# Kernel tuning notes

Hardware: AMD Instinct MI355X
Metric: run time of the kernel (lower is better)

## Reference

```python
import jax, jax.numpy as jnp
import numpy as np

M_COMP = 8      # number of output components m (n = m * tmax)
TMAX = 512
BS = 32
N = M_COMP * TMAX  # 4096


def setup_inputs() -> dict:
    key = jax.random.key(0)
    k1, k2, k3, k4 = jax.random.split(key, 4)
    # K must be symmetric positive definite for the Cholesky factorization.
    A = jax.random.normal(k1, (N, N), dtype=jnp.float32)
    K = A @ A.T / N + 1e-2 * jnp.eye(N, dtype=jnp.float32)
    # Sigma: diagonal measurement-noise covariance (positive diagonal).
    Sigma = jnp.diag(jax.random.uniform(k2, (N,), dtype=jnp.float32, minval=0.1, maxval=0.5))
    mu = jax.random.normal(k3, (N,), dtype=jnp.float32)
    Y = jax.random.normal(k4, (BS * N,), dtype=jnp.float32)
    return {"Y": Y, "mu": mu, "K": K, "Sigma": Sigma, "bs": BS, "tmax": TMAX}


def reference(Y, mu, K, Sigma, bs, tmax):
    n = mu.shape[0]  # m * tmax
    KS = K + Sigma
    # Chol_inv: inv = L^{-T} L^{-1} = (K + Sigma)^{-1}
    L = jnp.linalg.cholesky(KS)
    Linv = jnp.linalg.inv(L)
    inv = Linv.T @ Linv  # [n, n]
    # Block-diagonal quadratic form == sum of per-trajectory quadratic forms.
    diff = mu[None, :] - Y.reshape(bs, n)  # [bs, n]
    quad = jnp.einsum('bi,ij,bj->', diff, inv, diff)
    # log det(K + Sigma); slogdet is the stable equivalent (det > 0 for SPD).
    _, logdet = jnp.linalg.slogdet(KS)
    lml = (-quad / (2.0 * bs)
           - 0.5 * logdet
           - 0.5 * tmax * jnp.log(jnp.asarray(2.0 * np.pi, dtype=KS.dtype)))
    return -lml
```

## Files before the change

kernel.cpp:

```cpp
#include <hip/hip_runtime.h>
#include <math.h>

#define Nn 4096
#define BSc 32
#define NB 128
#define NBP 132
#define NBB 32
#define NBLK 33
#define NK 32
#define TILE_ELEMS (NB * NB)
#define NTILES 561

typedef float f32x4 __attribute__((ext_vector_type(4)));
typedef short bf16x8 __attribute__((ext_vector_type(8)));

__device__ __forceinline__ size_t tile_off(int i, int j) {
  return ((size_t)(j * NBLK - (j * (j - 1)) / 2 + (i - j))) * TILE_ELEMS;
}

__device__ __forceinline__ unsigned short f2bf(float f) {
  union { float f; unsigned int u; } v; v.f = f;
  unsigned int r = v.u + 0x7fffu + ((v.u >> 16) & 1u);
  return (unsigned short)(r >> 16);
}
__device__ __forceinline__ float bf2f(unsigned short b) {
  union { unsigned int u; float f; } v; v.u = ((unsigned int)b) << 16;
  return v.f;
}

__global__ __launch_bounds__(256) void prep(const float* __restrict__ Y,
                                            const float* __restrict__ mu,
                                            const float* __restrict__ Kp,
                                            const float* __restrict__ Sg,
                                            float* __restrict__ W) {
  int bid = blockIdx.x;
  int j = 0;
  while (j + 1 < NBLK) {
    int nxt = (j + 1) * NBLK - ((j + 1) * j) / 2;
    if (bid < nxt) break;
    ++j;
  }
  int start = j * NBLK - (j * (j - 1)) / 2;
  int i = j + (bid - start);
  float* T = W + tile_off(i, j);
  int tid = threadIdx.x;
  for (int idx = tid; idx < TILE_ELEMS; idx += 256) {
    int li = idx >> 7, lj = idx & 127;
    int gr = i * NB + li, gc = j * NB + lj;
    float v = 0.0f;
    if (gr < Nn) {
      v = Kp[(size_t)gr * Nn + gc];
      if (gr == gc) v += Sg[(size_t)gr * Nn + gr];
    } else {
      int b = gr - Nn;
      if (b < BSc && gc < Nn) v = mu[gc] - Y[(size_t)b * Nn + gc];
    }
    T[idx] = v;
  }
}

__global__ __launch_bounds__(256) void potf2(float* __restrict__ W, int k) {
  __shared__ float T[NB][NBP];
  __shared__ float dinv_sh[NBB];
  float* G = W + tile_off(k, k);
  int tid = threadIdx.x;
  for (int idx = tid; idx < TILE_ELEMS / 4; idx += 256) {
    float4 v = ((const float4*)G)[idx];
    int r = idx >> 5, c = (idx & 31) * 4;
    *(float4*)&T[r][c] = v;
  }
  __syncthreads();
  int lane = tid & 63, wid = tid >> 6;
#pragma unroll 1
  for (int kb = 0; kb < 4; ++kb) {
    int o = kb * NBB;
    if (wid == 0) {
      int ii = lane & 31;
      float cc[NBB];
#pragma unroll
      for (int p = 0; p < NBB; ++p) cc[p] = T[o + ii][o + p];
#pragma unroll
      for (int j = 0; j < NBB; ++j) {
        float s = cc[j];
#pragma unroll
        for (int p = 0; p < NBB; ++p) {
          if (p < j) s -= cc[p] * __shfl(cc[p], j, 64);
        }
        float sj = __shfl(s, j, 64);
        float d = sqrtf(sj);
        if (ii == j) cc[j] = d;
        else if (ii > j) cc[j] = s / d;
      }
      if (lane < 32) {
#pragma unroll
        for (int p = 0; p < NBB; ++p) {
          if (p <= ii) T[o + ii][o + p] = cc[p];
        }
      }
    }
    __syncthreads();
    if (tid < NBB) dinv_sh[tid] = 1.0f / T[o + tid][o + tid];
    __syncthreads();
    int R = NB - o - NBB;
    if (R > 0) {
      if (tid < R) {
        int r = o + NBB + tid;
        float x[NBB];
#pragma unroll
        for (int p4 = 0; p4 < 8; ++p4) {
          float4 v = *(const float4*)&T[r][o + p4 * 4];
          x[p4 * 4] = v.x; x[p4 * 4 + 1] = v.y; x[p4 * 4 + 2] = v.z; x[p4 * 4 + 3] = v.w;
        }
#pragma unroll
        for (int j = 0; j < NBB; ++j) {
          float s = x[j];
#pragma unroll
          for (int p = 0; p < NBB; ++p) {
            if (p < j) s -= x[p] * T[o + j][o + p];
          }
          x[j] = s * dinv_sh[j];
        }
#pragma unroll
        for (int c4 = 0; c4 < 8; ++c4) {
          float4 w; w.x = x[c4 * 4]; w.y = x[c4 * 4 + 1]; w.z = x[c4 * 4 + 2]; w.w = x[c4 * 4 + 3];
          *(float4*)&T[r][o + c4 * 4] = w;
        }
      }
      __syncthreads();
      int TL = R >> 2;
      int ntile = TL * (TL + 1) / 2;
#pragma unroll 1
      for (int t = tid; t < ntile; t += 256) {
        int ti = (int)((sqrtf(8.0f * t + 1.0f) - 1.0f) * 0.5f);
        while ((ti + 1) * (ti + 2) / 2 <= t) ++ti;
        while (ti * (ti + 1) / 2 > t) --ti;
        int tj = t - ti * (ti + 1) / 2;
        int tr = o + NBB + ti * 4, tc = o + NBB + tj * 4;
        float acc[4][4];
#pragma unroll
        for (int m = 0; m < 4; ++m)
#pragma unroll
          for (int n = 0; n < 4; ++n) acc[m][n] = 0.0f;
#pragma unroll
        for (int p4 = 0; p4 < 8; ++p4) {
          float4 a[4], b[4];
#pragma unroll
          for (int m = 0; m < 4; ++m) a[m] = *(const float4*)&T[tr + m][o + p4 * 4];
#pragma unroll
          for (int n = 0; n < 4; ++n) b[n] = *(const float4*)&T[tc + n][o + p4 * 4];
#pragma unroll
          for (int m = 0; m < 4; ++m)
#pragma unroll
            for (int n = 0; n < 4; ++n)
              acc[m][n] += a[m].x * b[n].x + a[m].y * b[n].y + a[m].z * b[n].z + a[m].w * b[n].w;
        }
#pragma unroll
        for (int m = 0; m < 4; ++m)
#pragma unroll
          for (int n = 0; n < 4; ++n) T[tr + m][tc + n] -= acc[m][n];
      }
    }
    __syncthreads();
  }
  for (int idx = tid; idx < TILE_ELEMS; idx += 256) {
    int i = idx >> 7, j = idx & 127;
    if (j <= i) G[idx] = T[i][j];
  }
}

__global__ __launch_bounds__(256) void trsm(float* __restrict__ W,
                                            unsigned short* __restrict__ PH,
                                            unsigned short* __restrict__ PL,
                                            int k) {
  __shared__ float Td[NB][NBP];
  __shared__ float X[NB][NBP];
  __shared__ float dinv_sh[NB];
  int tid = threadIdx.x;
  int i = k + 1 + blockIdx.x;
  int rows = (i == NBLK - 1) ? BSc : NB;
  const float* Gd = W + tile_off(k, k);
  const float* Gx = W + tile_off(i, k);
  for (int idx = tid; idx < TILE_ELEMS / 4; idx += 256) {
    float4 v = ((const float4*)Gd)[idx];
    float4 u = ((const float4*)Gx)[idx];
    int r = idx >> 5, c = (idx & 31) * 4;
    *(float4*)&Td[r][c] = v;
    if (r >= rows) { u.x = 0.0f; u.y = 0.0f; u.z = 0.0f; u.w = 0.0f; }
    *(float4*)&X[r][c] = u;
  }
  __syncthreads();
  if (tid < NB) dinv_sh[tid] = 1.0f / Td[tid][tid];
  __syncthreads();
  int rtile = (tid >> 3) * 4;
  int ctile = (tid & 7) * 4;
#pragma unroll 1
  for (int jb = 0; jb < 4; ++jb) {
    int o = jb * NBB;
    if (jb > 0) {
      float acc[4][4];
#pragma unroll
      for (int m = 0; m < 4; ++m)
#pragma unroll
        for (int n = 0; n < 4; ++n) acc[m][n] = 0.0f;
#pragma unroll 1
      for (int p4 = 0; p4 < (o >> 2); ++p4) {
        float4 a[4], b[4];
#pragma unroll
        for (int m = 0; m < 4; ++m) a[m] = *(const float4*)&X[rtile + m][p4 * 4];
#pragma unroll
        for (int n = 0; n < 4; ++n) b[n] = *(const float4*)&Td[o + ctile + n][p4 * 4];
#pragma unroll
        for (int m = 0; m < 4; ++m)
#pragma unroll
          for (int n = 0; n < 4; ++n)
            acc[m][n] += a[m].x * b[n].x + a[m].y * b[n].y + a[m].z * b[n].z + a[m].w * b[n].w;
      }
#pragma unroll
      for (int m = 0; m < 4; ++m)
#pragma unroll
        for (int n = 0; n < 4; ++n) X[rtile + m][o + ctile + n] -= acc[m][n];
      __syncthreads();
    }
    if (tid < NB) {
      int r = tid;
      float x[NBB];
#pragma unroll
      for (int p4 = 0; p4 < 8; ++p4) {
        float4 v = *(const float4*)&X[r][o + p4 * 4];
        x[p4 * 4] = v.x; x[p4 * 4 + 1] = v.y; x[p4 * 4 + 2] = v.z; x[p4 * 4 + 3] = v.w;
      }
#pragma unroll
      for (int j = 0; j < NBB; ++j) {
        float s = x[j];
#pragma unroll
        for (int p = 0; p < NBB; ++p) {
          if (p < j) s -= x[p] * Td[o + j][o + p];
        }
        x[j] = s * dinv_sh[o + j];
      }
#pragma unroll
      for (int c4 = 0; c4 < 8; ++c4) {
        float4 w; w.x = x[c4 * 4]; w.y = x[c4 * 4 + 1]; w.z = x[c4 * 4 + 2]; w.w = x[c4 * 4 + 3];
        *(float4*)&X[r][o + c4 * 4] = w;
      }
    }
    __syncthreads();
  }
  int r = tid >> 1, hf = tid & 1;
  unsigned short* ph = PH + (size_t)i * TILE_ELEMS + (size_t)r * NB + hf * 64;
  unsigned short* pl = PL + (size_t)i * TILE_ELEMS + (size_t)r * NB + hf * 64;
#pragma unroll 1
  for (int ch = 0; ch < 8; ++ch) {
    unsigned short hb[8], lb[8];
#pragma unroll
    for (int e = 0; e < 8; ++e) {
      float v = X[r][hf * 64 + ch * 8 + e];
      unsigned short h = f2bf(v);
      hb[e] = h;
      lb[e] = f2bf(v - bf2f(h));
    }
    *reinterpret_cast<uint4*>(&ph[ch * 8]) = *reinterpret_cast<const uint4*>(hb);
    *reinterpret_cast<uint4*>(&pl[ch * 8]) = *reinterpret_cast<const uint4*>(lb);
  }
}

__global__ __launch_bounds__(256) void syrk(const unsigned short* __restrict__ PH,
                                            const unsigned short* __restrict__ PL,
                                            float* __restrict__ W, int k) {
  int i = k + 1 + blockIdx.x, j = k + 1 + blockIdx.y;
  if (i < j) return;
  const unsigned short* Ahg = PH + (size_t)i * TILE_ELEMS;
  const unsigned short* Alg = PL + (size_t)i * TILE_ELEMS;
  const unsigned short* Bhg = PH + (size_t)j * TILE_ELEMS;
  const unsigned short* Blg = PL + (size_t)j * TILE_ELEMS;
  float* C = W + tile_off(i, j);
  __shared__ unsigned short Ah[NB][40], Al[NB][40], Bh[NB][40], Bl[NB][40];
  int tid = threadIdx.x, lane = tid & 63, wid = tid >> 6;
  int wr = wid >> 1, wc = wid & 1, lm = lane & 15, lk = lane >> 4;
  f32x4 acc[4][4];
#pragma unroll
  for (int m = 0; m < 4; ++m)
#pragma unroll
    for (int n = 0; n < 4; ++n) acc[m][n] = (f32x4)0.0f;
  int r = tid >> 1, hf = tid & 1;
#pragma unroll 1
  for (int kb = 0; kb < 4; ++kb) {
    int kbase = kb * 32;
    if (kb) __syncthreads();
#pragma unroll
    for (int c = 0; c < 2; ++c) {
      int lc = (hf * 2 + c) * 8;
      int kc = kbase + lc;
      *reinterpret_cast<uint4*>(&Ah[r][lc]) = *reinterpret_cast<const uint4*>(&Ahg[(size_t)r * NB + kc]);
      *reinterpret_cast<uint4*>(&Al[r][lc]) = *reinterpret_cast<const uint4*>(&Alg[(size_t)r * NB + kc]);
      *reinterpret_cast<uint4*>(&Bh[r][lc]) = *reinterpret_cast<const uint4*>(&Bhg[(size_t)r * NB + kc]);
      *reinterpret_cast<uint4*>(&Bl[r][lc]) = *reinterpret_cast<const uint4*>(&Blg[(size_t)r * NB + kc]);
    }
    __syncthreads();
    bf16x8 ah[4], al[4], bh[4], bl[4];
#pragma unroll
    for (int mt = 0; mt < 4; ++mt) {
      int row = wr * 64 + mt * 16 + lm;
      ah[mt] = *reinterpret_cast<const bf16x8*>(&Ah[row][lk * 8]);
      al[mt] = *reinterpret_cast<const bf16x8*>(&Al[row][lk * 8]);
    }
#pragma unroll
    for (int nt = 0; nt < 4; ++nt) {
      int col = wc * 64 + nt * 16 + lm;
      bh[nt] = *reinterpret_cast<const bf16x8*>(&Bh[col][lk * 8]);
      bl[nt] = *reinterpret_cast<const bf16x8*>(&Bl[col][lk * 8]);
    }
#pragma unroll
    for (int mt = 0; mt < 4; ++mt)
#pragma unroll
      for (int nt = 0; nt < 4; ++nt) {
        acc[mt][nt] = __builtin_amdgcn_mfma_f32_16x16x32_bf16(ah[mt], bh[nt], acc[mt][nt], 0, 0, 0);
        acc[mt][nt] = __builtin_amdgcn_mfma_f32_16x16x32_bf16(al[mt], bh[nt], acc[mt][nt], 0, 0, 0);
        acc[mt][nt] = __builtin_amdgcn_mfma_f32_16x16x32_bf16(ah[mt], bl[nt], acc[mt][nt], 0, 0, 0);
      }
  }
#pragma unroll
  for (int mt = 0; mt < 4; ++mt)
#pragma unroll
    for (int nt = 0; nt < 4; ++nt) {
#pragma unroll
      for (int q = 0; q < 4; ++q) {
        int rr = wr * 64 + mt * 16 + lk * 4 + q;
        int cc = wc * 64 + nt * 16 + lm;
        C[rr * NB + cc] -= acc[mt][nt][q];
      }
    }
}

__global__ __launch_bounds__(256) void finalize(const float* __restrict__ W,
                                                const int* __restrict__ bsp,
                                                const int* __restrict__ tmaxp,
                                                float* __restrict__ out) {
  __shared__ float rl[4], rq[4];
  int tid = threadIdx.x;
  float lsum = 0.0f;
  for (int d = tid; d < Nn; d += 256) {
    int db = d >> 7, dl = d & 127;
    lsum += logf(W[tile_off(db, db) + (size_t)dl * NB + dl]);
  }
  float qsum = 0.0f;
  if (tid < BSc) qsum = W[tile_off(NBLK - 1, NBLK - 1) + (size_t)tid * NB + tid];
  for (int o = 32; o > 0; o >>= 1) {
    lsum += __shfl_down(lsum, o, 64);
    qsum += __shfl_down(qsum, o, 64);
  }
  int lane = tid & 63, wid = tid >> 6;
  if (lane == 0) { rl[wid] = lsum; rq[wid] = qsum; }
  __syncthreads();
  if (tid == 0) {
    float Lt = rl[0] + rl[1] + rl[2] + rl[3];
    float Qt = rq[0] + rq[1] + rq[2] + rq[3];
    float bsf = (float)bsp[0];
    float tmaxf = (float)tmaxp[0];
    out[0] = -Qt / (2.0f * bsf) + Lt + 0.5f * tmaxf * logf(6.283185307179586f);
  }
}

extern "C" void kernel_launch(void* const* d_in, const int* in_sizes, int n_in,
                              void* d_out, int out_size, void* d_ws, size_t ws_size,
                              hipStream_t stream) {
  const float* Y   = (const float*)d_in[0];
  const float* mu  = (const float*)d_in[1];
  const float* Kp  = (const float*)d_in[2];
  const float* Sg  = (const float*)d_in[3];
  const int*   bsp = (const int*)d_in[4];
  const int*   tmp_= (const int*)d_in[5];
  float* W = (float*)d_ws;
  unsigned short* PH = (unsigned short*)(W + (size_t)NTILES * TILE_ELEMS);
  unsigned short* PL = PH + (size_t)NBLK * TILE_ELEMS;
  float* out = (float*)d_out;

  prep<<<NTILES, 256, 0, stream>>>(Y, mu, Kp, Sg, W);

  for (int k = 0; k < NK; ++k) {
    potf2<<<1, 256, 0, stream>>>(W, k);
    int T = NBLK - (k + 1);
    trsm<<<T, 256, 0, stream>>>(W, PH, PL, k);
    dim3 g(T, T);
    syrk<<<g, 256, 0, stream>>>(PH, PL, W, k);
  }
  finalize<<<1, 256, 0, stream>>>(W, bsp, tmp_, out);
}
```

Measured before the change: 3.917 ms.

## Fuse next diagonal-block Cholesky into the syrk block that updates it

New measurement: 3.696 ms, median of 2. 1.06x faster.

```diff
diff --git a/kernel.cpp b/kernel.cpp
--- a/kernel.cpp
+++ b/kernel.cpp
@@ -10,6 +10,9 @@
 #define NK 32
 #define TILE_ELEMS (NB * NB)
 #define NTILES 561
+
+#define SM_DINV 67584
+#define SM_SIZE 67712
 
 typedef float f32x4 __attribute__((ext_vector_type(4)));
 typedef short bf16x8 __attribute__((ext_vector_type(8)));
@@ -59,17 +62,8 @@
   }
 }
 
-__global__ __launch_bounds__(256) void potf2(float* __restrict__ W, int k) {
-  __shared__ float T[NB][NBP];
-  __shared__ float dinv_sh[NBB];
-  float* G = W + tile_off(k, k);
-  int tid = threadIdx.x;
-  for (int idx = tid; idx < TILE_ELEMS / 4; idx += 256) {
-    float4 v = ((const float4*)G)[idx];
-    int r = idx >> 5, c = (idx & 31) * 4;
-    *(float4*)&T[r][c] = v;
-  }
-  __syncthreads();
+__device__ __forceinline__ void factor_lds(float (*T)[NBP], float* dinv_sh,
+                                           int tid) {
   int lane = tid & 63, wid = tid >> 6;
 #pragma unroll 1
   for (int kb = 0; kb < 4; ++kb) {
@@ -162,6 +156,21 @@
     }
     __syncthreads();
   }
+}
+
+__global__ __launch_bounds__(256) void potf2(float* __restrict__ W, int k) {
+  __shared__ __align__(16) unsigned char SMEM[SM_SIZE];
+  float (*T)[NBP] = (float (*)[NBP])SMEM;
+  float* dinv_sh = (float*)(SMEM + SM_DINV);
+  float* G = W + tile_off(k, k);
+  int tid = threadIdx.x;
+  for (int idx = tid; idx < TILE_ELEMS / 4; idx += 256) {
+    float4 v = ((const float4*)G)[idx];
+    int r = idx >> 5, c = (idx & 31) * 4;
+    *(float4*)&T[r][c] = v;
+  }
+  __syncthreads();
+  factor_lds(T, dinv_sh, tid);
   for (int idx = tid; idx < TILE_ELEMS; idx += 256) {
     int i = idx >> 7, j = idx & 127;
     if (j <= i) G[idx] = T[i][j];
@@ -269,12 +278,16 @@
                                             float* __restrict__ W, int k) {
   int i = k + 1 + blockIdx.x, j = k + 1 + blockIdx.y;
   if (i < j) return;
+  __shared__ __align__(16) unsigned char SMEM[SM_SIZE];
+  unsigned short (*Ah)[40] = (unsigned short (*)[40])(SMEM);
+  unsigned short (*Al)[40] = (unsigned short (*)[40])(SMEM + 10240);
+  unsigned short (*Bh)[40] = (unsigned short (*)[40])(SMEM + 20480);
+  unsigned short (*Bl)[40] = (unsigned short (*)[40])(SMEM + 30720);
   const unsigned short* Ahg = PH + (size_t)i * TILE_ELEMS;
   const unsigned short* Alg = PL + (size_t)i * TILE_ELEMS;
   const unsigned short* Bhg = PH + (size_t)j * TILE_ELEMS;
   const unsigned short* Blg = PL + (size_t)j * TILE_ELEMS;
   float* C = W + tile_off(i, j);
-  __shared__ unsigned short Ah[NB][40], Al[NB][40], Bh[NB][40], Bl[NB][40];
   int tid = threadIdx.x, lane = tid & 63, wid = tid >> 6;
   int wr = wid >> 1, wc = wid & 1, lm = lane & 15, lk = lane >> 4;
   f32x4 acc[4][4];
@@ -319,17 +332,47 @@
         acc[mt][nt] = __builtin_amdgcn_mfma_f32_16x16x32_bf16(ah[mt], bl[nt], acc[mt][nt], 0, 0, 0);
       }
   }
-#pragma unroll
-  for (int mt = 0; mt < 4; ++mt)
-#pragma unroll
-    for (int nt = 0; nt < 4; ++nt) {
-#pragma unroll
-      for (int q = 0; q < 4; ++q) {
-        int rr = wr * 64 + mt * 16 + lk * 4 + q;
-        int cc = wc * 64 + nt * 16 + lm;
-        C[rr * NB + cc] -= acc[mt][nt][q];
-      }
-    }
+  bool dofac = (blockIdx.x == 0 && blockIdx.y == 0 && i < NBLK - 1);
+  if (!dofac) {
+#pragma unroll
+    for (int mt = 0; mt < 4; ++mt)
+#pragma unroll
+      for (int nt = 0; nt < 4; ++nt) {
+#pragma unroll
+        for (int q = 0; q < 4; ++q) {
+          int rr = wr * 64 + mt * 16 + lk * 4 + q;
+          int cc = wc * 64 + nt * 16 + lm;
+          C[rr * NB + cc] -= acc[mt][nt][q];
+        }
+      }
+  } else {
+    __syncthreads();
+    float (*T)[NBP] = (float (*)[NBP])SMEM;
+    float* dinv_sh = (float*)(SMEM + SM_DINV);
+    for (int idx = tid; idx < TILE_ELEMS / 4; idx += 256) {
+      float4 v = ((const float4*)C)[idx];
+      int rr = idx >> 5, cc = (idx & 31) * 4;
+      *(float4*)&T[rr][cc] = v;
+    }
+    __syncthreads();
+#pragma unroll
+    for (int mt = 0; mt < 4; ++mt)
+#pragma unroll
+      for (int nt = 0; nt < 4; ++nt) {
+#pragma unroll
+        for (int q = 0; q < 4; ++q) {
+          int rr = wr * 64 + mt * 16 + lk * 4 + q;
+          int cc = wc * 64 + nt * 16 + lm;
+          T[rr][cc] -= acc[mt][nt][q];
+        }
+      }
+    __syncthreads();
+    factor_lds(T, dinv_sh, tid);
+    for (int idx = tid; idx < TILE_ELEMS; idx += 256) {
+      int rr = idx >> 7, cc = idx & 127;
+      if (cc <= rr) C[idx] = T[rr][cc];
+    }
+  }
 }
 
 __global__ __launch_bounds__(256) void finalize(const float* __restrict__ W,
@@ -376,9 +419,9 @@
   float* out = (float*)d_out;
 
   prep<<<NTILES, 256, 0, stream>>>(Y, mu, Kp, Sg, W);
+  potf2<<<1, 256, 0, stream>>>(W, 0);
 
   for (int k = 0; k < NK; ++k) {
-    potf2<<<1, 256, 0, stream>>>(W, k);
     int T = NBLK - (k + 1);
     trsm<<<T, 256, 0, stream>>>(W, PH, PL, k);
     dim3 g(T, T);
```
